# Optimization experiments

Measured on AMD Instinct MI355X. Metric: run time of the kernel, lower is better.

The kernel has to match this reference:

```python
import jax, jax.numpy as jnp
import numpy as np

B, N, L, H = 32, 1024, 512, 8  # batch, num_id, Input_len, num_head
EPS = 1e-5


def _ln(x, g, b):
    m = jnp.mean(x, axis=-1, keepdims=True)
    v = jnp.mean((x - m) ** 2, axis=-1, keepdims=True)
    return (x - m) / jnp.sqrt(v + EPS) * g + b


def setup_inputs() -> dict:
    key = jax.random.key(0)
    ks = iter(jax.random.split(key, 40))
    w = lambda shape, s=0.02: jax.random.normal(next(ks), shape, jnp.float32) * s
    inp = {"x": jax.random.normal(next(ks), (B, N, L), jnp.float32)}
    for p in ("t", "c"):  # Time_de_att and cross_de_att params (conv1d k=1 -> [L,L])
        inp[f"{p}_Wq"] = w((L, L)); inp[f"{p}_bq"] = w((L,))
        inp[f"{p}_Wk"] = w((L, L)); inp[f"{p}_bk"] = w((L,))
        inp[f"{p}_Wv"] = w((L, L)); inp[f"{p}_bv"] = w((L,))
        inp[f"{p}_Wo"] = w((L, L, 1, H)); inp[f"{p}_bo"] = w((L,))  # Conv2d kernel (1,H)
        inp[f"{p}_g"] = jnp.ones((L,), jnp.float32); inp[f"{p}_b"] = jnp.zeros((L,), jnp.float32)
    inp["s_Wq"] = w((N, N)); inp["s_bq"] = w((N,))
    inp["s_Wk"] = w((N, N)); inp["s_bk"] = w((N,))
    inp["s_Wv"] = w((N, N)); inp["s_bv"] = w((N,))
    inp["s_W1"] = w((1, H)); inp["s_b1"] = w((1,))
    return inp


def _conv1x1(x_cn, W, b):  # x_cn: [B,C,len], W: [O,C]
    return jnp.einsum('oc,bcn->bon', W, x_cn) + b[None, :, None]


def _de_att(xq_src, xkv_src, Wq, bq, Wk, bk, Wv, bv, Wo, bo, g, bt):
    # xq_src, xkv_src: [B,L,N] (channels-first, as after x.transpose(-2,-1))
    q = _conv1x1(xq_src, Wq, bq).transpose(0, 2, 1)   # [B,N,L]
    k = _conv1x1(xkv_src, Wk, bk)                     # [B,L,N]
    v = _conv1x1(xkv_src, Wv, bv).transpose(0, 2, 1)  # [B,N,L]
    kd = jnp.sqrt(jnp.float32(N) / H)                 # k.shape[-1] == num_id
    attn = jax.nn.softmax(jnp.matmul(q, k) / kd, axis=-1)  # [B,N,N]
    line = jnp.matmul(attn, v)                        # [B,N,L]
    # eval-mode: all heads identical -> Conv2d(1,H) combine == sum weights over head axis
    Wsum = Wo[:, :, 0, :].sum(-1)                     # [L,L]
    res = jnp.einsum('oc,bcn->bon', Wsum, line.transpose(0, 2, 1)) + bo[None, :, None]
    out = (xkv_src + res).transpose(0, 2, 1)          # [B,N,L]
    return _ln(out, g, bt)


def reference(x,
              t_Wq, t_bq, t_Wk, t_bk, t_Wv, t_bv, t_Wo, t_bo, t_g, t_b,
              c_Wq, c_bq, c_Wk, c_bk, c_Wv, c_bv, c_Wo, c_bo, c_g, c_b,
              s_Wq, s_bq, s_Wk, s_bk, s_Wv, s_bv, s_W1, s_b1):
    xt = x.transpose(0, 2, 1)  # [B,L,N]
    # Time_de_att (self-attention over nodes, time as channels)
    time_out = _de_att(xt, xt, t_Wq, t_bq, t_Wk, t_bk, t_Wv, t_bv, t_Wo, t_bo, t_g, t_b)  # [B,N,L]
    # space_att2 (attention over time, nodes as features)
    q = xt @ s_Wq.T + s_bq                          # [B,L,N]
    k = (xt @ s_Wk.T + s_bk).transpose(0, 2, 1)     # [B,N,L]
    v = xt @ s_Wv.T + s_bv                          # [B,L,N]
    kd = jnp.sqrt(jnp.float32(L) / H)               # k.shape[-1] == Input_len
    line = jnp.matmul(jax.nn.softmax(jnp.matmul(q, k) / kd, axis=-1), v)  # [B,L,N]
    space_out = (line * s_W1.sum() + s_b1[0]).transpose(0, 2, 1)          # [B,N,L]
    # cross_de_att: q from space_out, k/v + residual from time_out
    out = _de_att(space_out.transpose(0, 2, 1), time_out.transpose(0, 2, 1),
                  c_Wq, c_bq, c_Wk, c_bk, c_Wv, c_bv, c_Wo, c_bo, c_g, c_b)
    return out  # [B,N,L]
```

## Files before the change

kernel.cpp:

```cpp
#include <hip/hip_runtime.h>
#include <hip/hip_bf16.h>

typedef __bf16 bf16;
typedef __bf16 bf16x8 __attribute__((ext_vector_type(8)));
typedef __bf16 bf16x4 __attribute__((ext_vector_type(4)));
typedef __bf16 bf16x2 __attribute__((ext_vector_type(2)));
typedef float f32x4 __attribute__((ext_vector_type(4)));

#define BATCH 32
#define N_ID 1024
#define L_IN 512

static const long ACT_E = (long)BATCH * N_ID * L_IN;
static const long S_NL  = (long)N_ID * L_IN;
static const long S_TT  = (long)N_ID * N_ID;

__device__ __forceinline__ void gload16(const bf16* g, bf16* l)
{
    __builtin_amdgcn_global_load_lds((__attribute__((address_space(1))) void*)g,
                                     (__attribute__((address_space(3))) void*)l, 16, 0, 0);
}

#define VM3 asm volatile("s_waitcnt vmcnt(3)" ::: "memory")
#define VM9 asm volatile("s_waitcnt vmcnt(9)" ::: "memory")
#define VM0 asm volatile("s_waitcnt vmcnt(0)" ::: "memory")
#define BAR __builtin_amdgcn_s_barrier()

#define COMPUTE(CIDX) \
    { \
      const bf16* pa = ldsb + (CIDX) * 12288; \
      const bf16* pb = pa + 8192; \
      bf16x8 af[4], bfv[4]; \
_Pragma("unroll") \
      for (int i = 0; i < 4; ++i) \
        af[i] = *(const bf16x8*)(pa + (wm * 64 + i * 16 + fr) * 32 + slotk); \
_Pragma("unroll") \
      for (int j = 0; j < 4; ++j) \
        bfv[j] = *(const bf16x8*)(pb + (wn * 64 + j * 16 + fr) * 32 + slotk); \
      __builtin_amdgcn_s_setprio(1); \
_Pragma("unroll") \
      for (int i = 0; i < 4; ++i) \
_Pragma("unroll") \
        for (int j = 0; j < 4; ++j) \
          acc[i][j] = __builtin_amdgcn_mfma_f32_16x16x32_bf16(af[i], bfv[j], acc[i][j], 0, 0, 0); \
      __builtin_amdgcn_s_setprio(0); \
    }

#define STAGE(CIDX, KT) { stgA(ldsb + (CIDX) * 12288, KT); \
                          stgB(ldsb + (CIDX) * 12288 + 8192, KT); }

template<int EPI>
__global__ __launch_bounds__(512, 4)
void gemm3(const bf16* __restrict__ A, const bf16* __restrict__ Bm, void* __restrict__ Cout,
           const float* __restrict__ biasCol, const float* __restrict__ biasRow,
           const void* __restrict__ Res, const float* __restrict__ scal2,
           float scale, int K,
           long lda, long ldb, long ldc,
           long sA, long sB, long sC, long sRes, long sBR, long sVp, int nsl,
           unsigned gy, unsigned gxy, unsigned nwg)
{
    __shared__ __align__(16) bf16 ldsbuf[2 * 12288];
    bf16* ldsb = ldsbuf;

    unsigned id = blockIdx.x;
    {
        const unsigned q = nwg >> 3, r = nwg & 7;
        const unsigned xcd = id & 7, off = id >> 3;
        id = (xcd < r ? xcd * (q + 1) : r * (q + 1) + (xcd - r) * q) + off;
    }
    const unsigned bz = id / gxy;
    const unsigned rem = id - bz * gxy;
    const unsigned bx = rem / gy;
    const unsigned by = rem - bx * gy;

    const int t = threadIdx.x;
    const int w = t >> 6;
    const int lane = t & 63;
    const int fr = lane & 15;
    const int kg = lane >> 4;
    const int wm = w >> 1, wn = w & 1;
    const long z = bz;
    const long m0 = (long)bx * 256;
    const long n0 = (long)by * 128;
    const bf16* Ab = A + z * sA;
    const bf16* Bb = Bm + z * sB;

    const int srow = w * 16 + (lane >> 2);
    const int gc = (lane & 3) ^ ((lane >> 3) & 3);
    const int slotk = (kg ^ ((fr >> 1) & 3)) * 8;

    auto stgA = [&](bf16* dst, int kt) {
#pragma unroll
        for (int r = 0; r < 2; ++r) {
            const int row = r * 128 + srow;
            gload16(Ab + (m0 + row) * lda + kt * 32 + gc * 8, dst + row * 32 + (lane & 3) * 8);
        }
    };
    auto stgB = [&](bf16* dst, int kt) {
        gload16(Bb + (n0 + srow) * ldb + kt * 32 + gc * 8, dst + srow * 32 + (lane & 3) * 8);
    };

    f32x4 acc[4][4] = {};

    const int NT = K >> 5;
    STAGE(0, 0); STAGE(1, 1);

    for (int kt = 0; kt < NT - 1; ++kt) {
        VM3; BAR;
        COMPUTE(kt & 1);
        BAR;
        if (kt + 2 < NT) STAGE(kt & 1, kt + 2);
    }
    VM0; BAR;
    COMPUTE((NT - 1) & 1);

    float e0 = 0.f, e1 = 0.f;
    if constexpr (EPI == 8) { e0 = scal2[0]; e1 = scal2[1]; }

    float rs[16];
    if constexpr (EPI == 6) {
#pragma unroll
        for (int vv = 0; vv < 16; ++vv) rs[vv] = 0.f;
    }

#pragma unroll
    for (int i = 0; i < 4; ++i) {
        const long rb = m0 + wm * 64 + i * 16 + kg * 4;
#pragma unroll
        for (int j = 0; j < 4; ++j) {
            const long cc = n0 + wn * 64 + j * 16 + fr;
            float cinv = 0.f, vj = 0.f;
            if constexpr (EPI == 8) {
                float s = 0.f;
#pragma unroll
                for (int k8 = 0; k8 < 8; ++k8) s += biasCol[z * sBR + cc * 8 + k8];
                cinv = 1.f / s;
            }
            if constexpr (EPI == 6) vj = biasCol[z * sVp + cc];
#pragma unroll
            for (int r = 0; r < 4; ++r) {
                const long rr = rb + r;
                const float v = acc[i][j][r];
                const long idx = z * sC + rr * ldc + cc;
                if constexpr (EPI == 1)      ((bf16*)Cout)[idx] = (bf16)(v + biasRow[rr]);
                else if constexpr (EPI == 3) ((bf16*)Cout)[idx] = (bf16)v;
                else if constexpr (EPI == 6) {
                    const float e = __builtin_amdgcn_exp2f(v * scale + vj);
                    ((bf16*)Cout)[idx] = (bf16)e;
                    rs[i * 4 + r] += e;
                }
                else                  ((bf16*)Cout)[idx] = (bf16)(v * cinv * e0 + e1);
            }
        }
    }

    if constexpr (EPI == 6) {
#pragma unroll
        for (int vv = 0; vv < 16; ++vv) {
            rs[vv] += __shfl_xor(rs[vv], 1);
            rs[vv] += __shfl_xor(rs[vv], 2);
            rs[vv] += __shfl_xor(rs[vv], 4);
            rs[vv] += __shfl_xor(rs[vv], 8);
        }
        if (fr == 0) {
            float* Rs = (float*)biasRow + z * sBR;
            const int slot = (int)by * 2 + wn;
#pragma unroll
            for (int i = 0; i < 4; ++i)
#pragma unroll
                for (int r = 0; r < 4; ++r) {
                    const long rr = m0 + wm * 64 + i * 16 + kg * 4 + r;
                    Rs[rr * nsl + slot] = rs[i * 4 + r];
                }
        }
    }
}

template<int OUTF32>
__global__ __launch_bounds__(256, 2)
void pvln(const bf16* __restrict__ P, const bf16* __restrict__ V,
          void* __restrict__ Out,
          const float* __restrict__ biasP, const float* __restrict__ Rslots,
          const bf16* __restrict__ Res,
          const float* __restrict__ g, const float* __restrict__ beta,
          unsigned nwg)
{
    __shared__ __align__(16) bf16 lds[2][18432];
    __shared__ float red[64][4][2];

    unsigned id = blockIdx.x;
    {
        const unsigned q = nwg >> 3, r = nwg & 7;
        const unsigned xcd = id & 7, off = id >> 3;
        id = (xcd < r ? xcd * (q + 1) : r * (q + 1) + (xcd - r) * q) + off;
    }
    const long z = id >> 4;
    const int m0 = (int)(id & 15) * 64;

    const int t = threadIdx.x;
    const int w = t >> 6;
    const int lane = t & 63;
    const int fr = lane & 15;
    const int kg = lane >> 4;

    const bf16* Ab = P + z * S_TT + (long)m0 * 1024;
    const bf16* Bb = V + z * S_NL;

    const int srow = t >> 2;
    const int gc = (t & 3) ^ ((t >> 3) & 3);
    const int slotk = (kg ^ ((fr >> 1) & 3)) * 8;

    auto stg = [&](int buf, int kt) {
        gload16(Ab + (long)srow * 1024 + kt * 32 + gc * 8,
                &lds[buf][srow * 32 + (t & 3) * 8]);
#pragma unroll
        for (int p0 = 0; p0 < 8; ++p0) {
            const int row = p0 * 64 + srow;
            gload16(Bb + (long)row * 1024 + kt * 32 + gc * 8,
                    &lds[buf][2048 + row * 32 + (t & 3) * 8]);
        }
    };

    f32x4 acc[4][8] = {};

    stg(0, 0); stg(1, 1);
#define PVCOMP(CIDX) \
    { \
      const bf16* pa = &lds[CIDX][0]; \
      const bf16* pb = &lds[CIDX][2048]; \
      bf16x8 af[4], bfv[8]; \
_Pragma("unroll") \
      for (int i = 0; i < 4; ++i) \
        af[i] = *(const bf16x8*)(pa + (i * 16 + fr) * 32 + slotk); \
_Pragma("unroll") \
      for (int j = 0; j < 8; ++j) \
        bfv[j] = *(const bf16x8*)(pb + (w * 128 + j * 16 + fr) * 32 + slotk); \
      __builtin_amdgcn_s_setprio(1); \
_Pragma("unroll") \
      for (int i = 0; i < 4; ++i) \
_Pragma("unroll") \
        for (int j = 0; j < 8; ++j) \
          acc[i][j] = __builtin_amdgcn_mfma_f32_16x16x32_bf16(af[i], bfv[j], acc[i][j], 0, 0, 0); \
      __builtin_amdgcn_s_setprio(0); \
    }

    for (int kt = 0; kt < 31; ++kt) {
        VM9; BAR;
        PVCOMP(kt & 1);
        BAR;
        if (kt + 2 < 32) stg(kt & 1, kt + 2);
    }
    VM0; BAR;
    PVCOMP(1);

    float rin[16];
#pragma unroll
    for (int i = 0; i < 4; ++i)
#pragma unroll
        for (int r = 0; r < 4; ++r) {
            float s = Rslots[z * 16384 + (long)(m0 + i * 16 + kg * 4 + r) * 16 + fr];
            s += __shfl_xor(s, 1); s += __shfl_xor(s, 2);
            s += __shfl_xor(s, 4); s += __shfl_xor(s, 8);
            rin[i * 4 + r] = 1.f / s;
        }

    float s1[16] = {}, s2[16] = {};
#pragma unroll
    for (int i = 0; i < 4; ++i)
#pragma unroll
        for (int j = 0; j < 8; ++j) {
            const int col = w * 128 + j * 16 + fr;
            const float bp = biasP[col];
#pragma unroll
            for (int r = 0; r < 4; ++r) {
                const int row = i * 16 + kg * 4 + r;
                float v = acc[i][j][r] * rin[i * 4 + r]
                        + (float)Res[z * S_NL + (long)(m0 + row) * 512 + col] + bp;
                acc[i][j][r] = v;
                s1[i * 4 + r] += v;
                s2[i * 4 + r] += v * v;
            }
        }

#pragma unroll
    for (int vv = 0; vv < 16; ++vv) {
        s1[vv] += __shfl_xor(s1[vv], 1); s2[vv] += __shfl_xor(s2[vv], 1);
        s1[vv] += __shfl_xor(s1[vv], 2); s2[vv] += __shfl_xor(s2[vv], 2);
        s1[vv] += __shfl_xor(s1[vv], 4); s2[vv] += __shfl_xor(s2[vv], 4);
        s1[vv] += __shfl_xor(s1[vv], 8); s2[vv] += __shfl_xor(s2[vv], 8);
    }
    __syncthreads();
    if (fr == 0) {
#pragma unroll
        for (int i = 0; i < 4; ++i)
#pragma unroll
            for (int r = 0; r < 4; ++r) {
                const int row = i * 16 + kg * 4 + r;
                red[row][w][0] = s1[i * 4 + r];
                red[row][w][1] = s2[i * 4 + r];
            }
    }
    __syncthreads();

    float mean[16], rstd[16];
#pragma unroll
    for (int i = 0; i < 4; ++i)
#pragma unroll
        for (int r = 0; r < 4; ++r) {
            const int row = i * 16 + kg * 4 + r;
            const float S1 = red[row][0][0] + red[row][1][0] + red[row][2][0] + red[row][3][0];
            const float S2 = red[row][0][1] + red[row][1][1] + red[row][2][1] + red[row][3][1];
            const float m = S1 * (1.f / 512.f);
            mean[i * 4 + r] = m;
            rstd[i * 4 + r] = rsqrtf(S2 * (1.f / 512.f) - m * m + 1e-5f);
        }

#pragma unroll
    for (int i = 0; i < 4; ++i)
#pragma unroll
        for (int j = 0; j < 8; ++j) {
            const int col = w * 128 + j * 16 + fr;
            const float gg = g[col], bb = beta[col];
#pragma unroll
            for (int r = 0; r < 4; ++r) {
                const int row = i * 16 + kg * 4 + r;
                const float o = (acc[i][j][r] - mean[i * 4 + r]) * rstd[i * 4 + r] * gg + bb;
                const long idx = (z * 1024 + m0 + row) * 512 + col;
                if constexpr (OUTF32) ((float*)Out)[idx] = o;
                else                  ((bf16*)Out)[idx] = (bf16)o;
            }
        }
}

__global__ __launch_bounds__(256)
void transpose_cvt(const float* __restrict__ x, bf16* __restrict__ Xb, bf16* __restrict__ xt)
{
    __shared__ bf16 tile[32][33];
    const int b = blockIdx.z;
    const int n0 = blockIdx.x * 32, l0 = blockIdx.y * 32;
    const long base = (long)b * N_ID * L_IN;
    const int tx = threadIdx.x, ty = threadIdx.y;
#pragma unroll
    for (int i = ty; i < 32; i += 8) {
        const long idx = base + (long)(n0 + i) * L_IN + l0 + tx;
        const bf16 s = (bf16)x[idx];
        Xb[idx] = s;
        tile[i][tx] = s;
    }
    __syncthreads();
#pragma unroll
    for (int i = ty; i < 32; i += 8)
        xt[base + (long)(l0 + i) * N_ID + n0 + tx] = tile[tx][i];
}

struct T6 { const float* s[6]; bf16* d[6]; };

__global__ __launch_bounds__(256)
void transpose512_6(T6 p)
{
    __shared__ bf16 tile[32][33];
    const float* src = p.s[blockIdx.z];
    bf16* dst = p.d[blockIdx.z];
    const int c0 = blockIdx.x * 32, r0 = blockIdx.y * 32;
    const int tx = threadIdx.x, ty = threadIdx.y;
#pragma unroll
    for (int i = ty; i < 32; i += 8)
        tile[i][tx] = (bf16)src[(long)(r0 + i) * 512 + c0 + tx];
    __syncthreads();
#pragma unroll
    for (int i = ty; i < 32; i += 8)
        dst[(long)(c0 + i) * 512 + r0 + tx] = tile[tx][i];
}

template<int N>
__global__ __launch_bounds__(256)
void transpose_mat(const float* __restrict__ a, const float* __restrict__ b,
                   bf16* __restrict__ da, bf16* __restrict__ db)
{
    __shared__ bf16 tile[32][33];
    const float* src = blockIdx.z ? b : a;
    bf16* dst = blockIdx.z ? db : da;
    const int c0 = blockIdx.x * 32, r0 = blockIdx.y * 32;
    const int tx = threadIdx.x, ty = threadIdx.y;
#pragma unroll
    for (int i = ty; i < 32; i += 8)
        tile[i][tx] = (bf16)src[(long)(r0 + i) * N + c0 + tx];
    __syncthreads();
#pragma unroll
    for (int i = ty; i < 32; i += 8)
        dst[(long)(c0 + i) * N + r0 + tx] = tile[tx][i];
}

__global__ void cvt_one(const float* __restrict__ s, bf16* __restrict__ d, int n)
{
    const int i = (blockIdx.x * 256 + threadIdx.x) * 4;
    if (i < n) {
        f32x4 v = *(const f32x4*)(s + i);
        bf16x4 o; o[0] = (bf16)v[0]; o[1] = (bf16)v[1]; o[2] = (bf16)v[2]; o[3] = (bf16)v[3];
        *(bf16x4*)(d + i) = o;
    }
}

__global__ void wo_sum2(const float* __restrict__ a, const float* __restrict__ b,
                        bf16* __restrict__ da, bf16* __restrict__ db)
{
    const int i = blockIdx.x * 256 + threadIdx.x;
    const float* src = blockIdx.y ? b : a;
    bf16* dst = blockIdx.y ? db : da;
    const float* p = src + (long)i * 8;
    float s = 0.f;
#pragma unroll
    for (int h = 0; h < 8; ++h) s += p[h];
    dst[i] = (bf16)s;
}

__global__ __launch_bounds__(64)
void biasfold2(const bf16* __restrict__ WsA, const float* __restrict__ bvA, const float* __restrict__ boA, float* __restrict__ outA,
               const bf16* __restrict__ WsB, const float* __restrict__ bvB, const float* __restrict__ boB, float* __restrict__ outB)
{
    const bf16* Ws = blockIdx.y ? WsB : WsA;
    const float* bv = blockIdx.y ? bvB : bvA;
    const float* bo = blockIdx.y ? boB : boA;
    float* out = blockIdx.y ? outB : outA;
    const int o = blockIdx.x;
    float s = 0.f;
    for (int l = threadIdx.x; l < 512; l += 64)
        s += (float)Ws[(long)o * 512 + l] * bv[l];
#pragma unroll
    for (int off = 32; off > 0; off >>= 1) s += __shfl_xor(s, off);
    if (threadIdx.x == 0) out[o] = bo[o] + s;
}

__global__ __launch_bounds__(64)
void vbarfold(const bf16* WkTrT, const float* tbq, float* vbarT,
              const bf16* WkTrC, const float* cbq, float* vbarC,
              const bf16* sWkTr, const float* sbq, float* vbarS,
              const float* sW1, const float* sb1, float* scal)
{
    const int o = blockIdx.x;
    const int y = blockIdx.y;
    if (y == 3) {
        if (o == 0 && threadIdx.x == 0) {
            float s = 0.f;
            for (int h = 0; h < 8; ++h) s += sW1[h];
            scal[0] = s; scal[1] = sb1[0];
        }
        return;
    }
    const bf16* W; const float* b; float* out; int D;
    if (y == 0)      { if (o >= 512) return; W = WkTrT; b = tbq; out = vbarT; D = 512; }
    else if (y == 1) { if (o >= 512) return; W = WkTrC; b = cbq; out = vbarC; D = 512; }
    else             { W = sWkTr; b = sbq; out = vbarS; D = 1024; }
    float s = 0.f;
    for (int a = threadIdx.x; a < D; a += 64)
        s += (float)W[(long)o * D + a] * b[a];
#pragma unroll
    for (int off = 32; off > 0; off >>= 1) s += __shfl_xor(s, off);
    if (threadIdx.x == 0) out[o] = s;
}

__global__ __launch_bounds__(256)
void vrow2(const bf16* __restrict__ Xb, const float* __restrict__ vbT, float* __restrict__ outT, float scT,
           const bf16* __restrict__ xt, const float* __restrict__ vbS, float* __restrict__ outS, float scS)
{
    const int lane = threadIdx.x & 63;
    if (blockIdx.y == 0) {
        const long row = (long)blockIdx.x * 4 + (threadIdx.x >> 6);
        const bf16* r = Xb + row * 512;
        bf16x8 xv = *(const bf16x8*)(r + lane * 8);
        const float* vb = vbT + lane * 8;
        float s = 0.f;
#pragma unroll
        for (int e = 0; e < 8; ++e) s += (float)xv[e] * vb[e];
#pragma unroll
        for (int o = 32; o > 0; o >>= 1) s += __shfl_xor(s, o);
        if (lane == 0) outT[row] = s * scT;
    } else {
        if (blockIdx.x >= 4096) return;
        const long row = (long)blockIdx.x * 4 + (threadIdx.x >> 6);
        const bf16* r = xt + row * 1024;
        float s = 0.f;
#pragma unroll
        for (int u = 0; u < 2; ++u) {
            bf16x8 xv = *(const bf16x8*)(r + u * 512 + lane * 8);
            const float* vb = vbS + u * 512 + lane * 8;
#pragma unroll
            for (int e = 0; e < 8; ++e) s += (float)xv[e] * vb[e];
        }
#pragma unroll
        for (int o = 32; o > 0; o >>= 1) s += __shfl_xor(s, o);
        if (lane == 0) outS[row] = s * scS;
    }
}

template<int D>
__global__ __launch_bounds__(256)
void vrow(const bf16* __restrict__ Src, const float* __restrict__ vbar,
          float* __restrict__ out, float scale2)
{
    const long row = (long)blockIdx.x * 4 + (threadIdx.x >> 6);
    const int lane = threadIdx.x & 63;
    const bf16* r = Src + row * D;
    float s = 0.f;
#pragma unroll
    for (int u = 0; u < D / 512; ++u) {
        bf16x8 xv = *(const bf16x8*)(r + u * 512 + lane * 8);
        const float* vb = vbar + u * 512 + lane * 8;
#pragma unroll
        for (int e = 0; e < 8; ++e) s += (float)xv[e] * vb[e];
    }
#pragma unroll
    for (int o = 32; o > 0; o >>= 1) s += __shfl_xor(s, o);
    if (lane == 0) out[row] = s * scale2;
}

static void launch_gemm(int epi, const bf16* A, const bf16* B, void* C,
                        const float* bc, const float* br, const void* res, const float* sc2,
                        float scale, int M, int N, int K,
                        long lda, long ldb, long ldc,
                        long sA, long sB, long sC, long sRes, long sBR, long sVp, int nsl,
                        int batches, hipStream_t st)
{
    const unsigned gx = M / 256, gy = N / 128;
    const unsigned gxy = gx * gy, nwg = gxy * (unsigned)batches;
    dim3 g(nwg), blk(512);
    switch (epi) {
    case 1: gemm3<1><<<g, blk, 0, st>>>(A, B, C, bc, br, res, sc2, scale, K, lda, ldb, ldc, sA, sB, sC, sRes, sBR, sVp, nsl, gy, gxy, nwg); break;
    case 3: gemm3<3><<<g, blk, 0, st>>>(A, B, C, bc, br, res, sc2, scale, K, lda, ldb, ldc, sA, sB, sC, sRes, sBR, sVp, nsl, gy, gxy, nwg); break;
    case 6: gemm3<6><<<g, blk, 0, st>>>(A, B, C, bc, br, res, sc2, scale, K, lda, ldb, ldc, sA, sB, sC, sRes, sBR, sVp, nsl, gy, gxy, nwg); break;
    default: gemm3<8><<<g, blk, 0, st>>>(A, B, C, bc, br, res, sc2, scale, K, lda, ldb, ldc, sA, sB, sC, sRes, sBR, sVp, nsl, gy, gxy, nwg); break;
    }
}

extern "C" void kernel_launch(void* const* d_in, const int* in_sizes, int n_in,
                              void* d_out, int out_size, void* d_ws, size_t ws_size,
                              hipStream_t stream)
{
    (void)in_sizes; (void)n_in; (void)out_size;

    const float* x   = (const float*)d_in[0];
    const float* tWq = (const float*)d_in[1];  const float* tbq = (const float*)d_in[2];
    const float* tWk = (const float*)d_in[3];
    const float* tWv = (const float*)d_in[5];  const float* tbv = (const float*)d_in[6];
    const float* tWo = (const float*)d_in[7];  const float* tbo = (const float*)d_in[8];
    const float* tg  = (const float*)d_in[9];  const float* tb  = (const float*)d_in[10];
    const float* cWq = (const float*)d_in[11]; const float* cbq = (const float*)d_in[12];
    const float* cWk = (const float*)d_in[13];
    const float* cWv = (const float*)d_in[15]; const float* cbv = (const float*)d_in[16];
    const float* cWo = (const float*)d_in[17]; const float* cbo = (const float*)d_in[18];
    const float* cg  = (const float*)d_in[19]; const float* cb  = (const float*)d_in[20];
    const float* sWq = (const float*)d_in[21]; const float* sbq = (const float*)d_in[22];
    const float* sWk = (const float*)d_in[23];
    const float* sWv = (const float*)d_in[25]; const float* sbv = (const float*)d_in[26];
    const float* sW1 = (const float*)d_in[27]; const float* sb1 = (const float*)d_in[28];

    char* p = (char*)d_ws;
    auto alloc = [&](size_t bytes) -> char* {
        char* r = p; p += (bytes + 255) & ~(size_t)255; return r;
    };

    bf16* WsT   = (bf16*)alloc(262144 * 2);
    bf16* WsC   = (bf16*)alloc(262144 * 2);
    bf16* WkTrT = (bf16*)alloc(262144 * 2);
    bf16* WkTrC = (bf16*)alloc(262144 * 2);
    bf16* WvTrT = (bf16*)alloc(262144 * 2);
    bf16* WvTrC = (bf16*)alloc(262144 * 2);
    bf16* WqTrT = (bf16*)alloc(262144 * 2);
    bf16* WqTrC = (bf16*)alloc(262144 * 2);
    bf16* WvWT  = (bf16*)alloc(262144 * 2);
    bf16* WvWC  = (bf16*)alloc(262144 * 2);
    bf16* MTt   = (bf16*)alloc(262144 * 2);
    bf16* MTc   = (bf16*)alloc(262144 * 2);
    bf16* sWqTr = (bf16*)alloc(1048576 * 2);
    bf16* sWkTr = (bf16*)alloc(1048576 * 2);
    bf16* MTs   = (bf16*)alloc(1048576 * 2);
    bf16* WvS   = (bf16*)alloc(1048576 * 2);
    float* scal  = (float*)alloc(256);
    float* biasT = (float*)alloc(512 * 4);
    float* biasC = (float*)alloc(512 * 4);
    float* vbarT = (float*)alloc(512 * 4);
    float* vbarC = (float*)alloc(512 * 4);
    float* vbarS = (float*)alloc(1024 * 4);

    const size_t ACT_B = (size_t)ACT_E * 2;
    bf16* bufG = (bf16*)alloc(ACT_B);
    bf16* Xb   = (bf16*)alloc(ACT_B);
    bf16* TO   = (bf16*)alloc(ACT_B);
    bf16* xt   = (bf16*)alloc(ACT_B);
    bf16* bufV = (bf16*)alloc(ACT_B);
    float* vpreT = (float*)alloc(BATCH * 1024 * 4);
    float* vpreS = (float*)alloc(BATCH * 512 * 4);
    float* Rbuf = (float*)alloc((size_t)BATCH * 1024 * 16 * 4);

    size_t used = (size_t)(p - (char*)d_ws);
    int CB = 32;
    while (CB > 1 && used + (size_t)CB * 2097152ULL + 4096 > ws_size) CB >>= 1;
    bf16* Sbuf = (bf16*)alloc((size_t)CB * 2097152ULL);
    bf16* Pbuf = Sbuf;

    const float L2E = 1.4426950408889634f;
    const float rsc_t2 = 0.08838834764831845f * L2E;
    const float rsc_s2 = 0.125f * L2E;

    T6 tj;
    tj.s[0] = tWv; tj.s[1] = cWv; tj.s[2] = tWq; tj.s[3] = cWq; tj.s[4] = tWk; tj.s[5] = cWk;
    tj.d[0] = WvTrT; tj.d[1] = WvTrC; tj.d[2] = WqTrT; tj.d[3] = WqTrC; tj.d[4] = WkTrT; tj.d[5] = WkTrC;
    transpose512_6<<<dim3(16, 16, 6), dim3(32, 8), 0, stream>>>(tj);
    transpose_mat<1024><<<dim3(32, 32, 2), dim3(32, 8), 0, stream>>>(sWq, sWk, sWqTr, sWkTr);
    cvt_one<<<dim3(1024), dim3(256), 0, stream>>>(sWv, WvS, 1048576);
    wo_sum2<<<dim3(1024, 2), dim3(256), 0, stream>>>(tWo, cWo, WsT, WsC);
    biasfold2<<<dim3(512, 2), dim3(64), 0, stream>>>(WsT, tbv, tbo, biasT, WsC, cbv, cbo, biasC);
    vbarfold<<<dim3(1024, 4), dim3(64), 0, stream>>>(WkTrT, tbq, vbarT, WkTrC, cbq, vbarC,
                                                     sWkTr, sbq, vbarS, sW1, sb1, scal);
    launch_gemm(3, WsT, WvTrT, WvWT, nullptr, nullptr, nullptr, nullptr, 0.f,
                512, 512, 512, 512, 512, 512, 262144, 262144, 262144, 0, 0, 0, 0, 4, stream);
    launch_gemm(3, sWkTr, sWqTr, MTs, nullptr, nullptr, nullptr, nullptr, 0.f,
                1024, 1024, 1024, 1024, 1024, 1024, 0, 0, 0, 0, 0, 0, 0, 1, stream);
    transpose_cvt<<<dim3(32, 16, BATCH), dim3(32, 8), 0, stream>>>(x, Xb, xt);
    vrow2<<<dim3(8192, 2), dim3(256), 0, stream>>>(Xb, vbarT, vpreT, rsc_t2, xt, vbarS, vpreS, rsc_s2);

    launch_gemm(3, Xb, MTt, bufG, nullptr, nullptr, nullptr, nullptr, 0.f,
                32768, 512, 512, 512, 512, 512, 0, 0, 0, 0, 0, 0, 0, 1, stream);
    launch_gemm(3, WvWT, Xb, bufV, nullptr, nullptr, nullptr, nullptr, 0.f,
                512, 1024, 512, 512, 512, 1024, 0, S_NL, S_NL, 0, 0, 0, 0, BATCH, stream);
    for (int c0 = 0; c0 < BATCH; c0 += CB) {
        const long off = (long)c0 * S_NL;
        launch_gemm(6, bufG + off, Xb + off, Sbuf, vpreT + (long)c0 * 1024, Rbuf, nullptr, nullptr, rsc_t2,
                    1024, 1024, 512, 512, 512, 1024, S_NL, S_NL, S_TT, 0, 16384, 1024, 16, CB, stream);
        pvln<0><<<dim3(CB * 16), dim3(256), 0, stream>>>(Sbuf, bufV + off, TO + off,
                                                         biasT, Rbuf, Xb + off, tg, tb, CB * 16);
    }

    bf16* SOp = Xb;
    launch_gemm(3, xt, MTs, bufG, nullptr, nullptr, nullptr, nullptr, 0.f,
                16384, 1024, 1024, 1024, 1024, 1024, 0, 0, 0, 0, 0, 0, 0, 1, stream);
    launch_gemm(1, WvS, xt, bufV, nullptr, sbv, nullptr, nullptr, 0.f,
                1024, 512, 1024, 1024, 1024, 512, 0, S_NL, S_NL, 0, 0, 0, 0, BATCH, stream);
    for (int c0 = 0; c0 < BATCH; c0 += CB) {
        const long off = (long)c0 * S_NL;
        launch_gemm(6, bufG + off, xt + off, Sbuf, vpreS + (long)c0 * 512, Rbuf, nullptr, nullptr, rsc_s2,
                    512, 512, 1024, 1024, 1024, 512, S_NL, S_NL, (long)L_IN * L_IN, 0, 4096, 512, 8, CB, stream);
        launch_gemm(8, bufV + off, Pbuf, SOp + off, Rbuf, nullptr, nullptr, scal, 0.f,
                    1024, 512, 512, 512, 512, 512, S_NL, (long)L_IN * L_IN, S_NL, 0, 4096, 0, 8, CB, stream);
    }

    launch_gemm(3, Xb, MTc, bufG, nullptr, nullptr, nullptr, nullptr, 0.f,
                32768, 512, 512, 512, 512, 512, 0, 0, 0, 0, 0, 0, 0, 1, stream);
    launch_gemm(3, WvWC, TO, bufV, nullptr, nullptr, nullptr, nullptr, 0.f,
                512, 1024, 512, 512, 512, 1024, 0, S_NL, S_NL, 0, 0, 0, 0, BATCH, stream);
    vrow<512><<<dim3(8192), dim3(256), 0, stream>>>(TO, vbarC, vpreT, rsc_t2);
    for (int c0 = 0; c0 < BATCH; c0 += CB) {
        const long off = (long)c0 * S_NL;
        launch_gemm(6, bufG + off, TO + off, Sbuf, vpreT + (long)c0 * 1024, Rbuf, nullptr, nullptr, rsc_t2,
                    1024, 1024, 512, 512, 512, 1024, S_NL, S_NL, S_TT, 0, 16384, 1024, 16, CB, stream);
        pvln<1><<<dim3(CB * 16), dim3(256), 0, stream>>>(Sbuf, bufV + off, (float*)d_out + off,
                                                         biasC, Rbuf, TO + off, cg, cb, CB * 16);
    }
}
```

Measured before the change: 630.9 us.

## Split pvln across 8 waves with 2x4 wave grid to cut accumulator registers

```diff
diff --git a/kernel.cpp b/kernel.cpp
--- a/kernel.cpp
+++ b/kernel.cpp
@@ -22,7 +22,7 @@
 }
 
 #define VM3 asm volatile("s_waitcnt vmcnt(3)" ::: "memory")
-#define VM9 asm volatile("s_waitcnt vmcnt(9)" ::: "memory")
+#define VM5 asm volatile("s_waitcnt vmcnt(5)" ::: "memory")
 #define VM0 asm volatile("s_waitcnt vmcnt(0)" ::: "memory")
 #define BAR __builtin_amdgcn_s_barrier()
 
@@ -177,7 +177,7 @@
 }
 
 template<int OUTF32>
-__global__ __launch_bounds__(256, 2)
+__global__ __launch_bounds__(512, 4)
 void pvln(const bf16* __restrict__ P, const bf16* __restrict__ V,
           void* __restrict__ Out,
           const float* __restrict__ biasP, const float* __restrict__ Rslots,
@@ -186,7 +186,7 @@
           unsigned nwg)
 {
     __shared__ __align__(16) bf16 lds[2][18432];
-    __shared__ float red[64][4][2];
+    __shared__ float red[64][5][2];
 
     unsigned id = blockIdx.x;
     {
@@ -202,50 +202,60 @@
     const int lane = t & 63;
     const int fr = lane & 15;
     const int kg = lane >> 4;
+    const int wm = w >> 2;
+    const int wn = w & 3;
 
     const bf16* Ab = P + z * S_TT + (long)m0 * 1024;
     const bf16* Bb = V + z * S_NL;
 
-    const int srow = t >> 2;
-    const int gc = (t & 3) ^ ((t >> 3) & 3);
+    const int srowB = t >> 2;
+    const int gcB = (t & 3) ^ ((t >> 3) & 3);
+    const int gcA = (lane & 3) ^ (lane >> 3);
     const int slotk = (kg ^ ((fr >> 1) & 3)) * 8;
 
     auto stg = [&](int buf, int kt) {
-        gload16(Ab + (long)srow * 1024 + kt * 32 + gc * 8,
-                &lds[buf][srow * 32 + (t & 3) * 8]);
-#pragma unroll
-        for (int p0 = 0; p0 < 8; ++p0) {
-            const int row = p0 * 64 + srow;
-            gload16(Bb + (long)row * 1024 + kt * 32 + gc * 8,
+        if (lane < 32) {
+            const int row = w * 8 + (lane >> 2);
+            gload16(Ab + (long)row * 1024 + kt * 32 + gcA * 8,
+                    &lds[buf][row * 32 + (lane & 3) * 8]);
+        }
+#pragma unroll
+        for (int p0 = 0; p0 < 4; ++p0) {
+            const int row = p0 * 128 + srowB;
+            gload16(Bb + (long)row * 1024 + kt * 32 + gcB * 8,
                     &lds[buf][2048 + row * 32 + (t & 3) * 8]);
         }
     };
 
-    f32x4 acc[4][8] = {};
-
-    stg(0, 0); stg(1, 1);
+    f32x4 acc[2][8] = {};
+
 #define PVCOMP(CIDX) \
     { \
       const bf16* pa = &lds[CIDX][0]; \
       const bf16* pb = &lds[CIDX][2048]; \
-      bf16x8 af[4], bfv[8]; \
-_Pragma("unroll") \
-      for (int i = 0; i < 4; ++i) \
-        af[i] = *(const bf16x8*)(pa + (i * 16 + fr) * 32 + slotk); \
-_Pragma("unroll") \
-      for (int j = 0; j < 8; ++j) \
-        bfv[j] = *(const bf16x8*)(pb + (w * 128 + j * 16 + fr) * 32 + slotk); \
-      __builtin_amdgcn_s_setprio(1); \
-_Pragma("unroll") \
-      for (int i = 0; i < 4; ++i) \
-_Pragma("unroll") \
-        for (int j = 0; j < 8; ++j) \
-          acc[i][j] = __builtin_amdgcn_mfma_f32_16x16x32_bf16(af[i], bfv[j], acc[i][j], 0, 0, 0); \
-      __builtin_amdgcn_s_setprio(0); \
-    }
-
+      bf16x8 af[2]; \
+_Pragma("unroll") \
+      for (int i = 0; i < 2; ++i) \
+        af[i] = *(const bf16x8*)(pa + (wm * 32 + i * 16 + fr) * 32 + slotk); \
+_Pragma("unroll") \
+      for (int jh = 0; jh < 2; ++jh) { \
+        bf16x8 bfv[4]; \
+_Pragma("unroll") \
+        for (int jj = 0; jj < 4; ++jj) \
+          bfv[jj] = *(const bf16x8*)(pb + (wn * 128 + (jh * 4 + jj) * 16 + fr) * 32 + slotk); \
+        __builtin_amdgcn_s_setprio(1); \
+_Pragma("unroll") \
+        for (int i = 0; i < 2; ++i) \
+_Pragma("unroll") \
+          for (int jj = 0; jj < 4; ++jj) \
+            acc[i][jh * 4 + jj] = __builtin_amdgcn_mfma_f32_16x16x32_bf16(af[i], bfv[jj], acc[i][jh * 4 + jj], 0, 0, 0); \
+        __builtin_amdgcn_s_setprio(0); \
+      } \
+    }
+
+    stg(0, 0); stg(1, 1);
     for (int kt = 0; kt < 31; ++kt) {
-        VM9; BAR;
+        VM5; BAR;
         PVCOMP(kt & 1);
         BAR;
         if (kt + 2 < 32) stg(kt & 1, kt + 2);
@@ -253,27 +263,27 @@
     VM0; BAR;
     PVCOMP(1);
 
-    float rin[16];
-#pragma unroll
-    for (int i = 0; i < 4; ++i)
+    float rin[8];
+#pragma unroll
+    for (int i = 0; i < 2; ++i)
 #pragma unroll
         for (int r = 0; r < 4; ++r) {
-            float s = Rslots[z * 16384 + (long)(m0 + i * 16 + kg * 4 + r) * 16 + fr];
+            float s = Rslots[z * 16384 + (long)(m0 + wm * 32 + i * 16 + kg * 4 + r) * 16 + fr];
             s += __shfl_xor(s, 1); s += __shfl_xor(s, 2);
             s += __shfl_xor(s, 4); s += __shfl_xor(s, 8);
             rin[i * 4 + r] = 1.f / s;
         }
 
-    float s1[16] = {}, s2[16] = {};
-#pragma unroll
-    for (int i = 0; i < 4; ++i)
+    float s1[8] = {}, s2[8] = {};
+#pragma unroll
+    for (int i = 0; i < 2; ++i)
 #pragma unroll
         for (int j = 0; j < 8; ++j) {
-            const int col = w * 128 + j * 16 + fr;
+            const int col = wn * 128 + j * 16 + fr;
             const float bp = biasP[col];
 #pragma unroll
             for (int r = 0; r < 4; ++r) {
-                const int row = i * 16 + kg * 4 + r;
+                const int row = wm * 32 + i * 16 + kg * 4 + r;
                 float v = acc[i][j][r] * rin[i * 4 + r]
                         + (float)Res[z * S_NL + (long)(m0 + row) * 512 + col] + bp;
                 acc[i][j][r] = v;
@@ -283,7 +293,7 @@
         }
 
 #pragma unroll
-    for (int vv = 0; vv < 16; ++vv) {
+    for (int vv = 0; vv < 8; ++vv) {
         s1[vv] += __shfl_xor(s1[vv], 1); s2[vv] += __shfl_xor(s2[vv], 1);
         s1[vv] += __shfl_xor(s1[vv], 2); s2[vv] += __shfl_xor(s2[vv], 2);
         s1[vv] += __shfl_xor(s1[vv], 4); s2[vv] += __shfl_xor(s2[vv], 4);
@@ -292,22 +302,22 @@
     __syncthreads();
     if (fr == 0) {
 #pragma unroll
-        for (int i = 0; i < 4; ++i)
+        for (int i = 0; i < 2; ++i)
 #pragma unroll
             for (int r = 0; r < 4; ++r) {
-                const int row = i * 16 + kg * 4 + r;
-                red[row][w][0] = s1[i * 4 + r];
-                red[row][w][1] = s2[i * 4 + r];
+                const int row = wm * 32 + i * 16 + kg * 4 + r;
+                red[row][wn][0] = s1[i * 4 + r];
+                red[row][wn][1] = s2[i * 4 + r];
             }
     }
     __syncthreads();
 
-    float mean[16], rstd[16];
-#pragma unroll
-    for (int i = 0; i < 4; ++i)
+    float mean[8], rstd[8];
+#pragma unroll
+    for (int i = 0; i < 2; ++i)
 #pragma unroll
         for (int r = 0; r < 4; ++r) {
-            const int row = i * 16 + kg * 4 + r;
+            const int row = wm * 32 + i * 16 + kg * 4 + r;
             const float S1 = red[row][0][0] + red[row][1][0] + red[row][2][0] + red[row][3][0];
             const float S2 = red[row][0][1] + red[row][1][1] + red[row][2][1] + red[row][3][1];
             const float m = S1 * (1.f / 512.f);
@@ -316,14 +326,14 @@
         }
 
 #pragma unroll
-    for (int i = 0; i < 4; ++i)
+    for (int i = 0; i < 2; ++i)
 #pragma unroll
         for (int j = 0; j < 8; ++j) {
-            const int col = w * 128 + j * 16 + fr;
+            const int col = wn * 128 + j * 16 + fr;
             const float gg = g[col], bb = beta[col];
 #pragma unroll
             for (int r = 0; r < 4; ++r) {
-                const int row = i * 16 + kg * 4 + r;
+                const int row = wm * 32 + i * 16 + kg * 4 + r;
                 const float o = (acc[i][j][r] - mean[i * 4 + r]) * rstd[i * 4 + r] * gg + bb;
                 const long idx = (z * 1024 + m0 + row) * 512 + col;
                 if constexpr (OUTF32) ((float*)Out)[idx] = o;
@@ -627,7 +637,7 @@
         const long off = (long)c0 * S_NL;
         launch_gemm(6, bufG + off, Xb + off, Sbuf, vpreT + (long)c0 * 1024, Rbuf, nullptr, nullptr, rsc_t2,
                     1024, 1024, 512, 512, 512, 1024, S_NL, S_NL, S_TT, 0, 16384, 1024, 16, CB, stream);
-        pvln<0><<<dim3(CB * 16), dim3(256), 0, stream>>>(Sbuf, bufV + off, TO + off,
+        pvln<0><<<dim3(CB * 16), dim3(512), 0, stream>>>(Sbuf, bufV + off, TO + off,
                                                          biasT, Rbuf, Xb + off, tg, tb, CB * 16);
     }
 
@@ -653,7 +663,7 @@
         const long off = (long)c0 * S_NL;
         launch_gemm(6, bufG + off, TO + off, Sbuf, vpreT + (long)c0 * 1024, Rbuf, nullptr, nullptr, rsc_t2,
                     1024, 1024, 512, 512, 512, 1024, S_NL, S_NL, S_TT, 0, 16384, 1024, 16, CB, stream);
-        pvln<1><<<dim3(CB * 16), dim3(256), 0, stream>>>(Sbuf, bufV + off, (float*)d_out + off,
+        pvln<1><<<dim3(CB * 16), dim3(512), 0, stream>>>(Sbuf, bufV + off, (float*)d_out + off,
                                                          biasC, Rbuf, TO + off, cg, cb, CB * 16);
     }
 }
```

Result: faster. 616.8 us (median of 2 runs) (-2.2%).
